# Performance work log

Measured on AMD Instinct MI355X. Metric: run time of the kernel, lower is better.

Reference implementation:

```python
import jax, jax.numpy as jnp
import numpy as np

N = 100000
E = 1600000
D = 128
EIG = 32
NUM_MOTIFS = 64
EPS = 1e-8  # torch cosine_similarity eps


def setup_inputs() -> dict:
    key = jax.random.key(0)
    ks = jax.random.split(key, 12)
    return {
        "q": jax.random.normal(ks[0], (N, D), jnp.float32),
        "k": jax.random.normal(ks[1], (N, D), jnp.float32),
        "v": jax.random.normal(ks[2], (N, D), jnp.float32),
        "eigs": jax.random.normal(ks[3], (N, EIG), jnp.float32),
        "motif_adj_vals": jax.random.uniform(ks[4], (E,), jnp.float32),
        "lambda0": jax.random.normal(ks[5], (1,), jnp.float32) * 0.1,
        "gamma": jax.random.normal(ks[6], (1,), jnp.float32) * 0.1,
        "motif_emb_w": jax.random.uniform(ks[7], (NUM_MOTIFS, 1), jnp.float32),
        "row": jax.random.randint(ks[8], (E,), 0, N, jnp.int32),
        "col": jax.random.randint(ks[9], (E,), 0, N, jnp.int32),
        "motif_ids": jax.random.randint(ks[10], (N,), 0, NUM_MOTIFS, jnp.int32),
    }


def _sparse_softmax(vals, row, n):
    # softmax of per-edge values grouped by destination/row index
    m = jax.ops.segment_max(vals, row, num_segments=n)
    e = jnp.exp(vals - m[row])
    z = jax.ops.segment_sum(e, row, num_segments=n)
    return e / z[row]


def reference(q, k, v, eigs, motif_adj_vals, lambda0, gamma, motif_emb_w,
              row, col, motif_ids):
    sqrt_dim = 1.0 / jnp.sqrt(jnp.asarray(q.shape[1], q.dtype))
    # edge-wise q.k dot product, scaled
    x = jnp.sum(q[row] * k[col], axis=-1) * sqrt_dim          # [E]
    # eig branch (args.model contains 'eig'); note original does NOT scale by sqrt_eig
    y = jnp.sum(eigs[row] * eigs[col], axis=-1)               # [E]
    s0 = x + jnp.exp(lambda0[0]) * y
    # motif branch: embedding lookup + cosine similarity along the edge dim (dim=0)
    me = motif_emb_w[motif_ids][:, 0]                          # [N]
    a, b = me[row], me[col]                                    # [E]
    sim = jnp.sum(a * b) / (jnp.maximum(jnp.linalg.norm(a), EPS)
                            * jnp.maximum(jnp.linalg.norm(b), EPS))
    s1 = motif_adj_vals * gamma[0] * sim                       # [E]
    n = q.shape[0]
    attn = 0.5 * (_sparse_softmax(s0, row, n) + _sparse_softmax(s1, row, n))
    # sparse-dense matmul: out[r] = sum_e attn_e * v[col_e]
    return jax.ops.segment_sum(attn[:, None] * v[col], row, num_segments=n)
```

## Files before the change

kernel.cpp:

```cpp
#include <hip/hip_runtime.h>
#include <math.h>

#define N_NODES 100000
#define N_EDGES 1600000
#define DIM 128
#define EIGD 32
#define CS_EPS 1e-8f

#define B1 256
#define CHUNK 6250
#define NB 391

static const size_t OFF_REC    = 0;
static const size_t OFF_SE     = 12800000;
static const size_t OFF_GH     = 25600000;
static const size_t OFF_BSTART = 26000384;
static const size_t OFF_GPART  = 26001952;
static const size_t OFF_OFFS   = 26006048;
static const size_t OFF_SCAL   = 26406064;
static const size_t OFF_KB     = 26406080;
static const size_t OFF_VB     = 52006080;
static const size_t OFF_EB     = 77606080;

__device__ __forceinline__ unsigned short f2bf(float f) {
    unsigned u = __float_as_uint(f);
    unsigned r = (u + 0x7fffu + ((u >> 16) & 1u)) >> 16;
    return (unsigned short)r;
}
__device__ __forceinline__ float blo(unsigned w) { return __uint_as_float(w << 16); }
__device__ __forceinline__ float bhi(unsigned w) { return __uint_as_float(w & 0xffff0000u); }

#define K4C 3200000
#define E4C 800000

__global__ void __launch_bounds__(256) ka_cvt(
        const float* __restrict__ k, const float* __restrict__ v,
        const float* __restrict__ eigs,
        ushort* __restrict__ kb, ushort* __restrict__ vb,
        ushort* __restrict__ eb) {
    int i = blockIdx.x * blockDim.x + threadIdx.x;
    const float* src; ushort* dst; int j;
    if (i < K4C)            { src = k;    dst = kb; j = i; }
    else if (i < 2 * K4C)   { src = v;    dst = vb; j = i - K4C; }
    else if (i < 2*K4C+E4C) { src = eigs; dst = eb; j = i - 2 * K4C; }
    else return;
    float4 f = ((const float4*)src)[j];
    ushort4 o;
    o.x = f2bf(f.x); o.y = f2bf(f.y); o.z = f2bf(f.z); o.w = f2bf(f.w);
    ((ushort4*)dst)[j] = o;
}

__global__ void __launch_bounds__(256) kb_hist(
        const int* __restrict__ row, const int* __restrict__ col,
        const float* __restrict__ motif_w, const int* __restrict__ motif_ids,
        int* __restrict__ gh, float4* __restrict__ gpart) {
    __shared__ int hist[NB];
    __shared__ float wlds[64];
    __shared__ float red[3][4];
    const int t = threadIdx.x, b = blockIdx.x;
    for (int i = t; i < NB; i += 256) hist[i] = 0;
    if (t < 64) wlds[t] = motif_w[t];
    __syncthreads();

    const int e0 = b * CHUNK, e1 = min(N_EDGES, e0 + CHUNK);
    float sab = 0.f, saa = 0.f, sbb = 0.f;
    for (int e = e0 + t; e < e1; e += 256) {
        int r = row[e], c = col[e];
        atomicAdd(&hist[r >> 8], 1);
        float mr = wlds[motif_ids[r]], mc = wlds[motif_ids[c]];
        sab += mr * mc; saa += mr * mr; sbb += mc * mc;
    }
#pragma unroll
    for (int off = 32; off >= 1; off >>= 1) {
        sab += __shfl_xor(sab, off);
        saa += __shfl_xor(saa, off);
        sbb += __shfl_xor(sbb, off);
    }
    int lane = t & 63, wid = t >> 6;
    if (lane == 0) { red[0][wid] = sab; red[1][wid] = saa; red[2][wid] = sbb; }
    __syncthreads();
    if (t == 0) {
        float a = 0.f, bb = 0.f, cc = 0.f;
#pragma unroll
        for (int i = 0; i < 4; i++) { a += red[0][i]; bb += red[1][i]; cc += red[2][i]; }
        gpart[b] = make_float4(a, bb, cc, 0.f);
    }
    __syncthreads();
    for (int i = t; i < NB; i += 256) gh[b * NB + i] = hist[i];
}

__global__ void __launch_bounds__(512) ke_scan(
        int* __restrict__ gh, int* __restrict__ bstart,
        const float4* __restrict__ gpart, const float* __restrict__ gamma,
        float* __restrict__ scal, int* __restrict__ offs) {
    const int t = threadIdx.x;
    __shared__ int tot[512];
    int mytot = 0;
    if (t < NB) {
        int run = 0;
        for (int b = 0; b < B1; b++) {
            int v = gh[b * NB + t];
            gh[b * NB + t] = run;
            run += v;
        }
        mytot = run;
    }
    tot[t] = mytot;
    __syncthreads();
    for (int off = 1; off < 512; off <<= 1) {
        int v = (t >= off) ? tot[t - off] : 0;
        __syncthreads();
        tot[t] += v;
        __syncthreads();
    }
    if (t < NB) bstart[t] = tot[t] - mytot;
    if (t == NB - 1) {
        bstart[NB] = tot[t];
        offs[N_NODES] = tot[t];
    }

    float sab = 0.f, saa = 0.f, sbb = 0.f;
    for (int i = t; i < B1; i += 512) {
        float4 g = gpart[i];
        sab += g.x; saa += g.y; sbb += g.z;
    }
#pragma unroll
    for (int off = 32; off >= 1; off >>= 1) {
        sab += __shfl_xor(sab, off);
        saa += __shfl_xor(saa, off);
        sbb += __shfl_xor(sbb, off);
    }
    __shared__ float red[3][8];
    int lane = t & 63, wid = t >> 6;
    if (lane == 0) { red[0][wid] = sab; red[1][wid] = saa; red[2][wid] = sbb; }
    __syncthreads();
    if (t == 0) {
        float a = 0.f, bb = 0.f, cc = 0.f;
#pragma unroll
        for (int i = 0; i < 8; i++) { a += red[0][i]; bb += red[1][i]; cc += red[2][i]; }
        float na = sqrtf(bb); if (na < CS_EPS) na = CS_EPS;
        float nb2 = sqrtf(cc); if (nb2 < CS_EPS) nb2 = CS_EPS;
        scal[0] = gamma[0] * (a / (na * nb2));
    }
}

__global__ void __launch_bounds__(256) kd_coarse(
        const int* __restrict__ row, const int* __restrict__ col,
        const float* __restrict__ adj, const int* __restrict__ gh,
        const int* __restrict__ bstart, int2* __restrict__ rec) {
    __shared__ int cur[NB];
    const int t = threadIdx.x, b = blockIdx.x;
    for (int i = t; i < NB; i += 256) cur[i] = bstart[i] + gh[b * NB + i];
    __syncthreads();
    const int e0 = b * CHUNK, e1 = min(N_EDGES, e0 + CHUNK);
    for (int e = e0 + t; e < e1; e += 256) {
        int r = row[e];
        int pos = atomicAdd(&cur[r >> 8], 1);
        rec[pos] = make_int2(col[e] | ((r & 255) << 17), __float_as_int(adj[e]));
    }
}

__global__ void __launch_bounds__(256) kf_fine(
        const int2* __restrict__ rec, const int* __restrict__ bstart,
        int* __restrict__ offs, float2* __restrict__ se) {
    __shared__ int hist[256], sc[256], cur[256];
    const int t = threadIdx.x, b = blockIdx.x;
    hist[t] = 0;
    __syncthreads();
    const int s = bstart[b], e1 = bstart[b + 1];
    for (int i = s + t; i < e1; i += 256) {
        int rl = (rec[i].x >> 17) & 255;
        atomicAdd(&hist[rl], 1);
    }
    __syncthreads();
    int v = hist[t];
    sc[t] = v;
    __syncthreads();
    for (int off = 1; off < 256; off <<= 1) {
        int w = (t >= off) ? sc[t - off] : 0;
        __syncthreads();
        sc[t] += w;
        __syncthreads();
    }
    int excl = sc[t] - v;
    int rowg = b * 256 + t;
    if (rowg < N_NODES) offs[rowg] = s + excl;
    cur[t] = s + excl;
    __syncthreads();
    for (int i = s + t; i < e1; i += 256) {
        int2 rc = rec[i];
        int rl = (rc.x >> 17) & 255;
        int pos = atomicAdd(&cur[rl], 1);
        se[pos] = make_float2(__int_as_float(rc.x & 0x1FFFF), __int_as_float(rc.y));
    }
}

__global__ void __launch_bounds__(256) k4_flash(
        const float* __restrict__ q, const ushort* __restrict__ kb,
        const ushort* __restrict__ eb, const ushort* __restrict__ vb,
        const float* __restrict__ lambda0, const int* __restrict__ offs,
        const float2* __restrict__ se, const float* __restrict__ scal,
        float* __restrict__ out) {
    const int tid  = threadIdx.x;
    const int lane = tid & 63;
    const int wid  = tid >> 6;
    const int r = blockIdx.x * 4 + wid;
    if (r >= N_NODES) return;
    const int l16 = lane & 15;
    const int grp = lane >> 4;
    const float inv_sqrt_d = 0.08838834764831843f;

    const int start = offs[r], end = offs[r + 1];
    if (end == start) {
        ((float2*)(out + (size_t)r * DIM))[lane] = make_float2(0.f, 0.f);
        return;
    }

    const float el0 = expf(lambda0[0]);
    const float cs  = scal[0];

    const float4* qp = (const float4*)(q + (size_t)r * DIM);
    const float4 qa = qp[l16 * 2];
    const float4 qc = qp[l16 * 2 + 1];
    const unsigned erw = *(const unsigned*)(eb + (size_t)r * EIGD + l16 * 2);
    const float er0 = blo(erw), er1 = bhi(erw);

    float m0 = -INFINITY, z0 = 0.f, m1 = -INFINITY, z1 = 0.f;
    float2 acc0 = make_float2(0.f, 0.f), acc1 = make_float2(0.f, 0.f);

    for (int base = start; base < end; base += 4) {
        int e = base + grp;
        float s0p = -INFINITY, s1v = -INFINITY;
        int c = 0;
        if (e < end) {
            float2 ea = se[e];
            c = __float_as_int(ea.x);
            s1v = cs * ea.y;
            const uint4 kw = *(const uint4*)(kb + (size_t)c * DIM + l16 * 8);
            float x;
            x = qa.x * blo(kw.x);
            x = fmaf(qa.y, bhi(kw.x), x);
            x = fmaf(qa.z, blo(kw.y), x);
            x = fmaf(qa.w, bhi(kw.y), x);
            x = fmaf(qc.x, blo(kw.z), x);
            x = fmaf(qc.y, bhi(kw.z), x);
            x = fmaf(qc.z, blo(kw.w), x);
            x = fmaf(qc.w, bhi(kw.w), x);
            const unsigned ecw = *(const unsigned*)(eb + (size_t)c * EIGD + l16 * 2);
            float y = er0 * blo(ecw) + er1 * bhi(ecw);
            s0p = x * inv_sqrt_d + el0 * y;
        }
#pragma unroll
        for (int off = 8; off >= 1; off >>= 1) s0p += __shfl_xor(s0p, off);

        float s00 = __shfl(s0p, 0),  s01 = __shfl(s0p, 16);
        float s02 = __shfl(s0p, 32), s03 = __shfl(s0p, 48);
        float s10 = __shfl(s1v, 0),  s11 = __shfl(s1v, 16);
        float s12 = __shfl(s1v, 32), s13 = __shfl(s1v, 48);
        int   c0  = __shfl(c, 0),    c1  = __shfl(c, 16);
        int   c2  = __shfl(c, 32),   c3  = __shfl(c, 48);
        int cnt = end - base;

        float nm0 = fmaxf(m0, fmaxf(fmaxf(s00, s01), fmaxf(s02, s03)));
        float r0  = __expf(m0 - nm0);
        float w00 = __expf(s00 - nm0);
        float w01 = __expf(s01 - nm0);
        float w02 = __expf(s02 - nm0);
        float w03 = __expf(s03 - nm0);
        z0 = z0 * r0 + w00 + w01 + w02 + w03;
        m0 = nm0;

        float nm1 = fmaxf(m1, fmaxf(fmaxf(s10, s11), fmaxf(s12, s13)));
        float r1  = __expf(m1 - nm1);
        float w10 = __expf(s10 - nm1);
        float w11 = __expf(s11 - nm1);
        float w12 = __expf(s12 - nm1);
        float w13 = __expf(s13 - nm1);
        z1 = z1 * r1 + w10 + w11 + w12 + w13;
        m1 = nm1;

        acc0.x *= r0; acc0.y *= r0;
        acc1.x *= r1; acc1.y *= r1;
        {
            unsigned vw = *(const unsigned*)(vb + (size_t)c0 * DIM + lane * 2);
            float vx = blo(vw), vy = bhi(vw);
            acc0.x = fmaf(w00, vx, acc0.x); acc0.y = fmaf(w00, vy, acc0.y);
            acc1.x = fmaf(w10, vx, acc1.x); acc1.y = fmaf(w10, vy, acc1.y);
        }
        if (cnt > 1) {
            unsigned vw = *(const unsigned*)(vb + (size_t)c1 * DIM + lane * 2);
            float vx = blo(vw), vy = bhi(vw);
            acc0.x = fmaf(w01, vx, acc0.x); acc0.y = fmaf(w01, vy, acc0.y);
            acc1.x = fmaf(w11, vx, acc1.x); acc1.y = fmaf(w11, vy, acc1.y);
        }
        if (cnt > 2) {
            unsigned vw = *(const unsigned*)(vb + (size_t)c2 * DIM + lane * 2);
            float vx = blo(vw), vy = bhi(vw);
            acc0.x = fmaf(w02, vx, acc0.x); acc0.y = fmaf(w02, vy, acc0.y);
            acc1.x = fmaf(w12, vx, acc1.x); acc1.y = fmaf(w12, vy, acc1.y);
        }
        if (cnt > 3) {
            unsigned vw = *(const unsigned*)(vb + (size_t)c3 * DIM + lane * 2);
            float vx = blo(vw), vy = bhi(vw);
            acc0.x = fmaf(w03, vx, acc0.x); acc0.y = fmaf(w03, vy, acc0.y);
            acc1.x = fmaf(w13, vx, acc1.x); acc1.y = fmaf(w13, vy, acc1.y);
        }
    }

    float iz0 = 1.f / z0, iz1 = 1.f / z1;
    float2 o = make_float2(0.5f * (acc0.x * iz0 + acc1.x * iz1),
                           0.5f * (acc0.y * iz0 + acc1.y * iz1));
    ((float2*)(out + (size_t)r * DIM))[lane] = o;
}

extern "C" void kernel_launch(void* const* d_in, const int* in_sizes, int n_in,
                              void* d_out, int out_size, void* d_ws, size_t ws_size,
                              hipStream_t stream) {
    const float* q        = (const float*)d_in[0];
    const float* k        = (const float*)d_in[1];
    const float* v        = (const float*)d_in[2];
    const float* eigs     = (const float*)d_in[3];
    const float* adj      = (const float*)d_in[4];
    const float* lambda0  = (const float*)d_in[5];
    const float* gamma    = (const float*)d_in[6];
    const float* motif_w  = (const float*)d_in[7];
    const int*   row      = (const int*)d_in[8];
    const int*   col      = (const int*)d_in[9];
    const int*   motif_ids= (const int*)d_in[10];
    float* out = (float*)d_out;

    char* ws = (char*)d_ws;
    int2*   rec    = (int2*)(ws + OFF_REC);
    float2* se     = (float2*)(ws + OFF_SE);
    int*    gh     = (int*)(ws + OFF_GH);
    int*    bstart = (int*)(ws + OFF_BSTART);
    float4* gpart  = (float4*)(ws + OFF_GPART);
    int*    offs   = (int*)(ws + OFF_OFFS);
    float*  scal   = (float*)(ws + OFF_SCAL);
    ushort* kb     = (ushort*)(ws + OFF_KB);
    ushort* vb     = (ushort*)(ws + OFF_VB);
    ushort* eb     = (ushort*)(ws + OFF_EB);

    hipLaunchKernelGGL(ka_cvt, dim3((2 * K4C + E4C + 255) / 256), dim3(256), 0, stream,
                       k, v, eigs, kb, vb, eb);
    hipLaunchKernelGGL(kb_hist, dim3(B1), dim3(256), 0, stream,
                       row, col, motif_w, motif_ids, gh, gpart);
    hipLaunchKernelGGL(ke_scan, dim3(1), dim3(512), 0, stream,
                       gh, bstart, gpart, gamma, scal, offs);
    hipLaunchKernelGGL(kd_coarse, dim3(B1), dim3(256), 0, stream,
                       row, col, adj, gh, bstart, rec);
    hipLaunchKernelGGL(kf_fine, dim3(NB), dim3(256), 0, stream,
                       rec, bstart, offs, se);
    hipLaunchKernelGGL(k4_flash, dim3((N_NODES + 3) / 4), dim3(256), 0, stream,
                       q, kb, eb, vb, lambda0, offs, se, scal, out);
}
```

Measured before the change: 478.1 us.

## Fuse fine bucket sort into attention kernel and parallelize histogram scan

```diff
diff --git a/kernel.cpp b/kernel.cpp
--- a/kernel.cpp
+++ b/kernel.cpp
@@ -7,20 +7,24 @@
 #define EIGD 32
 #define CS_EPS 1e-8f
 
-#define B1 256
-#define CHUNK 6250
-#define NB 391
+#define HB 1024
+#define CHUNK 1563
+#define NB2 1563
+#define CAP 1536
+#define K4C 3200000
+#define E4C 800000
+#define CVB 28125
 
 static const size_t OFF_REC    = 0;
-static const size_t OFF_SE     = 12800000;
-static const size_t OFF_GH     = 25600000;
-static const size_t OFF_BSTART = 26000384;
-static const size_t OFF_GPART  = 26001952;
-static const size_t OFF_OFFS   = 26006048;
-static const size_t OFF_SCAL   = 26406064;
-static const size_t OFF_KB     = 26406080;
-static const size_t OFF_VB     = 52006080;
-static const size_t OFF_EB     = 77606080;
+static const size_t OFF_GH     = 12800000;
+static const size_t OFF_BSTART = 19202048;
+static const size_t OFF_BTOT   = 19208304;
+static const size_t OFF_GPART  = 19214560;
+static const size_t OFF_FLAG   = 19230944;
+static const size_t OFF_SCAL   = 19230960;
+static const size_t OFF_KB     = 19231040;
+static const size_t OFF_VB     = 44831040;
+static const size_t OFF_EB     = 70431040;
 
 __device__ __forceinline__ unsigned short f2bf(float f) {
     unsigned u = __float_as_uint(f);
@@ -30,43 +34,38 @@
 __device__ __forceinline__ float blo(unsigned w) { return __uint_as_float(w << 16); }
 __device__ __forceinline__ float bhi(unsigned w) { return __uint_as_float(w & 0xffff0000u); }
 
-#define K4C 3200000
-#define E4C 800000
-
-__global__ void __launch_bounds__(256) ka_cvt(
+__global__ void __launch_bounds__(256) k1_cvt_hist(
         const float* __restrict__ k, const float* __restrict__ v,
         const float* __restrict__ eigs,
-        ushort* __restrict__ kb, ushort* __restrict__ vb,
-        ushort* __restrict__ eb) {
-    int i = blockIdx.x * blockDim.x + threadIdx.x;
-    const float* src; ushort* dst; int j;
-    if (i < K4C)            { src = k;    dst = kb; j = i; }
-    else if (i < 2 * K4C)   { src = v;    dst = vb; j = i - K4C; }
-    else if (i < 2*K4C+E4C) { src = eigs; dst = eb; j = i - 2 * K4C; }
-    else return;
-    float4 f = ((const float4*)src)[j];
-    ushort4 o;
-    o.x = f2bf(f.x); o.y = f2bf(f.y); o.z = f2bf(f.z); o.w = f2bf(f.w);
-    ((ushort4*)dst)[j] = o;
-}
-
-__global__ void __launch_bounds__(256) kb_hist(
         const int* __restrict__ row, const int* __restrict__ col,
         const float* __restrict__ motif_w, const int* __restrict__ motif_ids,
-        int* __restrict__ gh, float4* __restrict__ gpart) {
-    __shared__ int hist[NB];
+        ushort* __restrict__ kb, ushort* __restrict__ vb, ushort* __restrict__ eb,
+        int* __restrict__ gh, float4* __restrict__ gpart, int* __restrict__ flag) {
+    const int t = threadIdx.x, b = blockIdx.x;
+    if (b >= HB) {
+        int i = (b - HB) * 256 + t;
+        const float* src; ushort* dst; int j;
+        if (i < K4C)          { src = k;    dst = kb; j = i; }
+        else if (i < 2 * K4C) { src = v;    dst = vb; j = i - K4C; }
+        else                  { src = eigs; dst = eb; j = i - 2 * K4C; }
+        float4 f = ((const float4*)src)[j];
+        ushort4 o;
+        o.x = f2bf(f.x); o.y = f2bf(f.y); o.z = f2bf(f.z); o.w = f2bf(f.w);
+        ((ushort4*)dst)[j] = o;
+        return;
+    }
+    __shared__ int hist[NB2];
     __shared__ float wlds[64];
     __shared__ float red[3][4];
-    const int t = threadIdx.x, b = blockIdx.x;
-    for (int i = t; i < NB; i += 256) hist[i] = 0;
+    if (b == 0 && t == 0) flag[0] = 0;
+    for (int i = t; i < NB2; i += 256) hist[i] = 0;
     if (t < 64) wlds[t] = motif_w[t];
     __syncthreads();
-
     const int e0 = b * CHUNK, e1 = min(N_EDGES, e0 + CHUNK);
     float sab = 0.f, saa = 0.f, sbb = 0.f;
     for (int e = e0 + t; e < e1; e += 256) {
         int r = row[e], c = col[e];
-        atomicAdd(&hist[r >> 8], 1);
+        atomicAdd(&hist[r >> 6], 1);
         float mr = wlds[motif_ids[r]], mc = wlds[motif_ids[c]];
         sab += mr * mc; saa += mr * mr; sbb += mc * mc;
     }
@@ -85,96 +84,23 @@
         for (int i = 0; i < 4; i++) { a += red[0][i]; bb += red[1][i]; cc += red[2][i]; }
         gpart[b] = make_float4(a, bb, cc, 0.f);
     }
-    __syncthreads();
-    for (int i = t; i < NB; i += 256) gh[b * NB + i] = hist[i];
-}
-
-__global__ void __launch_bounds__(512) ke_scan(
-        int* __restrict__ gh, int* __restrict__ bstart,
+    for (int i = t; i < NB2; i += 256) gh[b * NB2 + i] = hist[i];
+}
+
+__global__ void __launch_bounds__(256) k2_scan(
+        int* __restrict__ gh, int* __restrict__ btot, int* __restrict__ bstart,
         const float4* __restrict__ gpart, const float* __restrict__ gamma,
-        float* __restrict__ scal, int* __restrict__ offs) {
-    const int t = threadIdx.x;
-    __shared__ int tot[512];
-    int mytot = 0;
-    if (t < NB) {
-        int run = 0;
-        for (int b = 0; b < B1; b++) {
-            int v = gh[b * NB + t];
-            gh[b * NB + t] = run;
-            run += v;
-        }
-        mytot = run;
-    }
-    tot[t] = mytot;
-    __syncthreads();
-    for (int off = 1; off < 512; off <<= 1) {
-        int v = (t >= off) ? tot[t - off] : 0;
-        __syncthreads();
-        tot[t] += v;
-        __syncthreads();
-    }
-    if (t < NB) bstart[t] = tot[t] - mytot;
-    if (t == NB - 1) {
-        bstart[NB] = tot[t];
-        offs[N_NODES] = tot[t];
-    }
-
-    float sab = 0.f, saa = 0.f, sbb = 0.f;
-    for (int i = t; i < B1; i += 512) {
-        float4 g = gpart[i];
-        sab += g.x; saa += g.y; sbb += g.z;
-    }
-#pragma unroll
-    for (int off = 32; off >= 1; off >>= 1) {
-        sab += __shfl_xor(sab, off);
-        saa += __shfl_xor(saa, off);
-        sbb += __shfl_xor(sbb, off);
-    }
-    __shared__ float red[3][8];
-    int lane = t & 63, wid = t >> 6;
-    if (lane == 0) { red[0][wid] = sab; red[1][wid] = saa; red[2][wid] = sbb; }
-    __syncthreads();
-    if (t == 0) {
-        float a = 0.f, bb = 0.f, cc = 0.f;
-#pragma unroll
-        for (int i = 0; i < 8; i++) { a += red[0][i]; bb += red[1][i]; cc += red[2][i]; }
-        float na = sqrtf(bb); if (na < CS_EPS) na = CS_EPS;
-        float nb2 = sqrtf(cc); if (nb2 < CS_EPS) nb2 = CS_EPS;
-        scal[0] = gamma[0] * (a / (na * nb2));
-    }
-}
-
-__global__ void __launch_bounds__(256) kd_coarse(
-        const int* __restrict__ row, const int* __restrict__ col,
-        const float* __restrict__ adj, const int* __restrict__ gh,
-        const int* __restrict__ bstart, int2* __restrict__ rec) {
-    __shared__ int cur[NB];
-    const int t = threadIdx.x, b = blockIdx.x;
-    for (int i = t; i < NB; i += 256) cur[i] = bstart[i] + gh[b * NB + i];
-    __syncthreads();
-    const int e0 = b * CHUNK, e1 = min(N_EDGES, e0 + CHUNK);
-    for (int e = e0 + t; e < e1; e += 256) {
-        int r = row[e];
-        int pos = atomicAdd(&cur[r >> 8], 1);
-        rec[pos] = make_int2(col[e] | ((r & 255) << 17), __float_as_int(adj[e]));
-    }
-}
-
-__global__ void __launch_bounds__(256) kf_fine(
-        const int2* __restrict__ rec, const int* __restrict__ bstart,
-        int* __restrict__ offs, float2* __restrict__ se) {
-    __shared__ int hist[256], sc[256], cur[256];
-    const int t = threadIdx.x, b = blockIdx.x;
-    hist[t] = 0;
-    __syncthreads();
-    const int s = bstart[b], e1 = bstart[b + 1];
-    for (int i = s + t; i < e1; i += 256) {
-        int rl = (rec[i].x >> 17) & 255;
-        atomicAdd(&hist[rl], 1);
-    }
-    __syncthreads();
-    int v = hist[t];
-    sc[t] = v;
+        float* __restrict__ scal, int* __restrict__ flag) {
+    const int t = threadIdx.x, cb = blockIdx.x;
+    __shared__ int sc[256];
+    __shared__ int lastf;
+    __shared__ float red[3][4];
+    int v0 = gh[(t * 4 + 0) * NB2 + cb];
+    int v1 = gh[(t * 4 + 1) * NB2 + cb];
+    int v2 = gh[(t * 4 + 2) * NB2 + cb];
+    int v3 = gh[(t * 4 + 3) * NB2 + cb];
+    int tot4 = v0 + v1 + v2 + v3;
+    sc[t] = tot4;
     __syncthreads();
     for (int off = 1; off < 256; off <<= 1) {
         int w = (t >= off) ? sc[t - off] : 0;
@@ -182,135 +108,223 @@
         sc[t] += w;
         __syncthreads();
     }
-    int excl = sc[t] - v;
-    int rowg = b * 256 + t;
-    if (rowg < N_NODES) offs[rowg] = s + excl;
-    cur[t] = s + excl;
-    __syncthreads();
-    for (int i = s + t; i < e1; i += 256) {
-        int2 rc = rec[i];
-        int rl = (rc.x >> 17) & 255;
-        int pos = atomicAdd(&cur[rl], 1);
-        se[pos] = make_float2(__int_as_float(rc.x & 0x1FFFF), __int_as_float(rc.y));
-    }
-}
-
-__global__ void __launch_bounds__(256) k4_flash(
+    int excl = sc[t] - tot4;
+    gh[(t * 4 + 0) * NB2 + cb] = excl;
+    gh[(t * 4 + 1) * NB2 + cb] = excl + v0;
+    gh[(t * 4 + 2) * NB2 + cb] = excl + v0 + v1;
+    gh[(t * 4 + 3) * NB2 + cb] = excl + v0 + v1 + v2;
+    if (t == 255) atomicExch(&btot[cb], excl + tot4);
+    __syncthreads();
+    if (t == 0) lastf = (atomicAdd(flag, 1) == NB2 - 1);
+    __syncthreads();
+    if (!lastf) return;
+
+    if (t < 64) {
+        int base = 0;
+        for (int ch = 0; ch < (NB2 + 63) / 64; ++ch) {
+            int idx = ch * 64 + t;
+            int vv = (idx < NB2) ? atomicAdd(&btot[idx], 0) : 0;
+            int inc = vv;
+#pragma unroll
+            for (int off = 1; off < 64; off <<= 1) {
+                int w = __shfl_up(inc, off);
+                if (t >= off) inc += w;
+            }
+            if (idx < NB2) bstart[idx] = base + inc - vv;
+            base += __shfl(inc, 63);
+        }
+        if (t == 0) bstart[NB2] = base;
+    }
+    float a2 = 0.f, b2 = 0.f, c2 = 0.f;
+    for (int i = t; i < HB; i += 256) {
+        float4 g = gpart[i];
+        a2 += g.x; b2 += g.y; c2 += g.z;
+    }
+#pragma unroll
+    for (int off = 32; off >= 1; off >>= 1) {
+        a2 += __shfl_xor(a2, off);
+        b2 += __shfl_xor(b2, off);
+        c2 += __shfl_xor(c2, off);
+    }
+    int lane = t & 63, wid = t >> 6;
+    if (lane == 0) { red[0][wid] = a2; red[1][wid] = b2; red[2][wid] = c2; }
+    __syncthreads();
+    if (t == 0) {
+        float a = 0.f, bb = 0.f, cc = 0.f;
+#pragma unroll
+        for (int i = 0; i < 4; i++) { a += red[0][i]; bb += red[1][i]; cc += red[2][i]; }
+        float na = sqrtf(bb); if (na < CS_EPS) na = CS_EPS;
+        float nb2v = sqrtf(cc); if (nb2v < CS_EPS) nb2v = CS_EPS;
+        scal[0] = gamma[0] * (a / (na * nb2v));
+    }
+}
+
+__global__ void __launch_bounds__(256) k3_coarse(
+        const int* __restrict__ row, const int* __restrict__ col,
+        const float* __restrict__ adj, const int* __restrict__ gh,
+        const int* __restrict__ bstart, int2* __restrict__ rec) {
+    __shared__ int cur[NB2];
+    const int t = threadIdx.x, b = blockIdx.x;
+    for (int i = t; i < NB2; i += 256) cur[i] = bstart[i] + gh[b * NB2 + i];
+    __syncthreads();
+    const int e0 = b * CHUNK, e1 = min(N_EDGES, e0 + CHUNK);
+    for (int e = e0 + t; e < e1; e += 256) {
+        int r = row[e];
+        int pos = atomicAdd(&cur[r >> 6], 1);
+        rec[pos] = make_int2(col[e] | ((r & 63) << 17), __float_as_int(adj[e]));
+    }
+}
+
+__global__ void __launch_bounds__(256) k4_flashf(
         const float* __restrict__ q, const ushort* __restrict__ kb,
         const ushort* __restrict__ eb, const ushort* __restrict__ vb,
-        const float* __restrict__ lambda0, const int* __restrict__ offs,
-        const float2* __restrict__ se, const float* __restrict__ scal,
+        const float* __restrict__ lambda0, const int* __restrict__ bstart,
+        const int2* __restrict__ rec, const float* __restrict__ scal,
         float* __restrict__ out) {
-    const int tid  = threadIdx.x;
-    const int lane = tid & 63;
-    const int wid  = tid >> 6;
-    const int r = blockIdx.x * 4 + wid;
-    if (r >= N_NODES) return;
-    const int l16 = lane & 15;
-    const int grp = lane >> 4;
-    const float inv_sqrt_d = 0.08838834764831843f;
-
-    const int start = offs[r], end = offs[r + 1];
-    if (end == start) {
-        ((float2*)(out + (size_t)r * DIM))[lane] = make_float2(0.f, 0.f);
-        return;
-    }
+    const int t = threadIdx.x, b = blockIdx.x;
+    const int lane = t & 63, wid = t >> 6;
+    const int l16 = lane & 15, grp = lane >> 4;
+    __shared__ int2 lrec[CAP];
+    __shared__ int2 srec[CAP];
+    __shared__ int lhist[64], lscan[64], lcur[64];
+
+    const int s = bstart[b];
+    int cnt = bstart[b + 1] - s;
+    if (cnt > CAP) cnt = CAP;
+    if (t < 64) lhist[t] = 0;
+    __syncthreads();
+    for (int i = t; i < cnt; i += 256) {
+        int2 rc = rec[s + i];
+        lrec[i] = rc;
+        atomicAdd(&lhist[(rc.x >> 17) & 63], 1);
+    }
+    __syncthreads();
+    if (t < 64) {
+        int h = lhist[t];
+        int inc = h;
+#pragma unroll
+        for (int off = 1; off < 64; off <<= 1) {
+            int w = __shfl_up(inc, off);
+            if (t >= off) inc += w;
+        }
+        lscan[t] = inc - h;
+        lcur[t]  = inc - h;
+    }
+    __syncthreads();
+    for (int i = t; i < cnt; i += 256) {
+        int2 rc = lrec[i];
+        int rl = (rc.x >> 17) & 63;
+        int p = atomicAdd(&lcur[rl], 1);
+        srec[p] = make_int2(rc.x & 0x1FFFF, rc.y);
+    }
+    __syncthreads();
 
     const float el0 = expf(lambda0[0]);
     const float cs  = scal[0];
-
-    const float4* qp = (const float4*)(q + (size_t)r * DIM);
-    const float4 qa = qp[l16 * 2];
-    const float4 qc = qp[l16 * 2 + 1];
-    const unsigned erw = *(const unsigned*)(eb + (size_t)r * EIGD + l16 * 2);
-    const float er0 = blo(erw), er1 = bhi(erw);
-
-    float m0 = -INFINITY, z0 = 0.f, m1 = -INFINITY, z1 = 0.f;
-    float2 acc0 = make_float2(0.f, 0.f), acc1 = make_float2(0.f, 0.f);
-
-    for (int base = start; base < end; base += 4) {
-        int e = base + grp;
-        float s0p = -INFINITY, s1v = -INFINITY;
-        int c = 0;
-        if (e < end) {
-            float2 ea = se[e];
-            c = __float_as_int(ea.x);
-            s1v = cs * ea.y;
-            const uint4 kw = *(const uint4*)(kb + (size_t)c * DIM + l16 * 8);
-            float x;
-            x = qa.x * blo(kw.x);
-            x = fmaf(qa.y, bhi(kw.x), x);
-            x = fmaf(qa.z, blo(kw.y), x);
-            x = fmaf(qa.w, bhi(kw.y), x);
-            x = fmaf(qc.x, blo(kw.z), x);
-            x = fmaf(qc.y, bhi(kw.z), x);
-            x = fmaf(qc.z, blo(kw.w), x);
-            x = fmaf(qc.w, bhi(kw.w), x);
-            const unsigned ecw = *(const unsigned*)(eb + (size_t)c * EIGD + l16 * 2);
-            float y = er0 * blo(ecw) + er1 * bhi(ecw);
-            s0p = x * inv_sqrt_d + el0 * y;
+    const float inv_sqrt_d = 0.08838834764831843f;
+
+    for (int rr = 0; rr < 16; ++rr) {
+        const int rloc = wid * 16 + rr;
+        const int r = b * 64 + rloc;
+        if (r >= N_NODES) break;
+        const int lst = lscan[rloc], led = lcur[rloc];
+        if (led == lst) {
+            ((float2*)(out + (size_t)r * DIM))[lane] = make_float2(0.f, 0.f);
+            continue;
         }
-#pragma unroll
-        for (int off = 8; off >= 1; off >>= 1) s0p += __shfl_xor(s0p, off);
-
-        float s00 = __shfl(s0p, 0),  s01 = __shfl(s0p, 16);
-        float s02 = __shfl(s0p, 32), s03 = __shfl(s0p, 48);
-        float s10 = __shfl(s1v, 0),  s11 = __shfl(s1v, 16);
-        float s12 = __shfl(s1v, 32), s13 = __shfl(s1v, 48);
-        int   c0  = __shfl(c, 0),    c1  = __shfl(c, 16);
-        int   c2  = __shfl(c, 32),   c3  = __shfl(c, 48);
-        int cnt = end - base;
-
-        float nm0 = fmaxf(m0, fmaxf(fmaxf(s00, s01), fmaxf(s02, s03)));
-        float r0  = __expf(m0 - nm0);
-        float w00 = __expf(s00 - nm0);
-        float w01 = __expf(s01 - nm0);
-        float w02 = __expf(s02 - nm0);
-        float w03 = __expf(s03 - nm0);
-        z0 = z0 * r0 + w00 + w01 + w02 + w03;
-        m0 = nm0;
-
-        float nm1 = fmaxf(m1, fmaxf(fmaxf(s10, s11), fmaxf(s12, s13)));
-        float r1  = __expf(m1 - nm1);
-        float w10 = __expf(s10 - nm1);
-        float w11 = __expf(s11 - nm1);
-        float w12 = __expf(s12 - nm1);
-        float w13 = __expf(s13 - nm1);
-        z1 = z1 * r1 + w10 + w11 + w12 + w13;
-        m1 = nm1;
-
-        acc0.x *= r0; acc0.y *= r0;
-        acc1.x *= r1; acc1.y *= r1;
-        {
-            unsigned vw = *(const unsigned*)(vb + (size_t)c0 * DIM + lane * 2);
-            float vx = blo(vw), vy = bhi(vw);
-            acc0.x = fmaf(w00, vx, acc0.x); acc0.y = fmaf(w00, vy, acc0.y);
-            acc1.x = fmaf(w10, vx, acc1.x); acc1.y = fmaf(w10, vy, acc1.y);
+        const float4* qp = (const float4*)(q + (size_t)r * DIM);
+        const float4 qa = qp[l16 * 2];
+        const float4 qc = qp[l16 * 2 + 1];
+        const unsigned erw = *(const unsigned*)(eb + (size_t)r * EIGD + l16 * 2);
+        const float er0 = blo(erw), er1 = bhi(erw);
+
+        float m0 = -INFINITY, z0 = 0.f, m1 = -INFINITY, z1 = 0.f;
+        float2 acc0 = make_float2(0.f, 0.f), acc1 = make_float2(0.f, 0.f);
+
+        for (int base = lst; base < led; base += 4) {
+            int e = base + grp;
+            float s0p = -INFINITY, s1v = -INFINITY;
+            int c = 0;
+            if (e < led) {
+                int2 ea = srec[e];
+                c = ea.x;
+                s1v = cs * __int_as_float(ea.y);
+                const uint4 kw = *(const uint4*)(kb + (size_t)c * DIM + l16 * 8);
+                float x;
+                x = qa.x * blo(kw.x);
+                x = fmaf(qa.y, bhi(kw.x), x);
+                x = fmaf(qa.z, blo(kw.y), x);
+                x = fmaf(qa.w, bhi(kw.y), x);
+                x = fmaf(qc.x, blo(kw.z), x);
+                x = fmaf(qc.y, bhi(kw.z), x);
+                x = fmaf(qc.z, blo(kw.w), x);
+                x = fmaf(qc.w, bhi(kw.w), x);
+                const unsigned ecw = *(const unsigned*)(eb + (size_t)c * EIGD + l16 * 2);
+                float y = er0 * blo(ecw) + er1 * bhi(ecw);
+                s0p = x * inv_sqrt_d + el0 * y;
+            }
+#pragma unroll
+            for (int off = 8; off >= 1; off >>= 1) s0p += __shfl_xor(s0p, off);
+
+            float s00 = __shfl(s0p, 0),  s01 = __shfl(s0p, 16);
+            float s02 = __shfl(s0p, 32), s03 = __shfl(s0p, 48);
+            float s10 = __shfl(s1v, 0),  s11 = __shfl(s1v, 16);
+            float s12 = __shfl(s1v, 32), s13 = __shfl(s1v, 48);
+            int   c0  = __shfl(c, 0),    c1  = __shfl(c, 16);
+            int   c2  = __shfl(c, 32),   c3  = __shfl(c, 48);
+            int rem = led - base;
+
+            float nm0 = fmaxf(m0, fmaxf(fmaxf(s00, s01), fmaxf(s02, s03)));
+            float r0  = __expf(m0 - nm0);
+            float w00 = __expf(s00 - nm0);
+            float w01 = __expf(s01 - nm0);
+            float w02 = __expf(s02 - nm0);
+            float w03 = __expf(s03 - nm0);
+            z0 = z0 * r0 + w00 + w01 + w02 + w03;
+            m0 = nm0;
+
+            float nm1 = fmaxf(m1, fmaxf(fmaxf(s10, s11), fmaxf(s12, s13)));
+            float r1  = __expf(m1 - nm1);
+            float w10 = __expf(s10 - nm1);
+            float w11 = __expf(s11 - nm1);
+            float w12 = __expf(s12 - nm1);
+            float w13 = __expf(s13 - nm1);
+            z1 = z1 * r1 + w10 + w11 + w12 + w13;
+            m1 = nm1;
+
+            acc0.x *= r0; acc0.y *= r0;
+            acc1.x *= r1; acc1.y *= r1;
+            {
+                unsigned vw = *(const unsigned*)(vb + (size_t)c0 * DIM + lane * 2);
+                float vx = blo(vw), vy = bhi(vw);
+                acc0.x = fmaf(w00, vx, acc0.x); acc0.y = fmaf(w00, vy, acc0.y);
+                acc1.x = fmaf(w10, vx, acc1.x); acc1.y = fmaf(w10, vy, acc1.y);
+            }
+            if (rem > 1) {
+                unsigned vw = *(const unsigned*)(vb + (size_t)c1 * DIM + lane * 2);
+                float vx = blo(vw), vy = bhi(vw);
+                acc0.x = fmaf(w01, vx, acc0.x); acc0.y = fmaf(w01, vy, acc0.y);
+                acc1.x = fmaf(w11, vx, acc1.x); acc1.y = fmaf(w11, vy, acc1.y);
+            }
+            if (rem > 2) {
+                unsigned vw = *(const unsigned*)(vb + (size_t)c2 * DIM + lane * 2);
+                float vx = blo(vw), vy = bhi(vw);
+                acc0.x = fmaf(w02, vx, acc0.x); acc0.y = fmaf(w02, vy, acc0.y);
+                acc1.x = fmaf(w12, vx, acc1.x); acc1.y = fmaf(w12, vy, acc1.y);
+            }
+            if (rem > 3) {
+                unsigned vw = *(const unsigned*)(vb + (size_t)c3 * DIM + lane * 2);
+                float vx = blo(vw), vy = bhi(vw);
+                acc0.x = fmaf(w03, vx, acc0.x); acc0.y = fmaf(w03, vy, acc0.y);
+                acc1.x = fmaf(w13, vx, acc1.x); acc1.y = fmaf(w13, vy, acc1.y);
+            }
         }
-        if (cnt > 1) {
-            unsigned vw = *(const unsigned*)(vb + (size_t)c1 * DIM + lane * 2);
-            float vx = blo(vw), vy = bhi(vw);
-            acc0.x = fmaf(w01, vx, acc0.x); acc0.y = fmaf(w01, vy, acc0.y);
-            acc1.x = fmaf(w11, vx, acc1.x); acc1.y = fmaf(w11, vy, acc1.y);
-        }
-        if (cnt > 2) {
-            unsigned vw = *(const unsigned*)(vb + (size_t)c2 * DIM + lane * 2);
-            float vx = blo(vw), vy = bhi(vw);
-            acc0.x = fmaf(w02, vx, acc0.x); acc0.y = fmaf(w02, vy, acc0.y);
-            acc1.x = fmaf(w12, vx, acc1.x); acc1.y = fmaf(w12, vy, acc1.y);
-        }
-        if (cnt > 3) {
-            unsigned vw = *(const unsigned*)(vb + (size_t)c3 * DIM + lane * 2);
-            float vx = blo(vw), vy = bhi(vw);
-            acc0.x = fmaf(w03, vx, acc0.x); acc0.y = fmaf(w03, vy, acc0.y);
-            acc1.x = fmaf(w13, vx, acc1.x); acc1.y = fmaf(w13, vy, acc1.y);
-        }
-    }
-
-    float iz0 = 1.f / z0, iz1 = 1.f / z1;
-    float2 o = make_float2(0.5f * (acc0.x * iz0 + acc1.x * iz1),
-                           0.5f * (acc0.y * iz0 + acc1.y * iz1));
-    ((float2*)(out + (size_t)r * DIM))[lane] = o;
+
+        float iz0 = 1.f / z0, iz1 = 1.f / z1;
+        float2 o = make_float2(0.5f * (acc0.x * iz0 + acc1.x * iz1),
+                               0.5f * (acc0.y * iz0 + acc1.y * iz1));
+        ((float2*)(out + (size_t)r * DIM))[lane] = o;
+    }
 }
 
 extern "C" void kernel_launch(void* const* d_in, const int* in_sizes, int n_in,
@@ -331,26 +345,23 @@
 
     char* ws = (char*)d_ws;
     int2*   rec    = (int2*)(ws + OFF_REC);
-    float2* se     = (float2*)(ws + OFF_SE);
     int*    gh     = (int*)(ws + OFF_GH);
     int*    bstart = (int*)(ws + OFF_BSTART);
+    int*    btot   = (int*)(ws + OFF_BTOT);
     float4* gpart  = (float4*)(ws + OFF_GPART);
-    int*    offs   = (int*)(ws + OFF_OFFS);
+    int*    flag   = (int*)(ws + OFF_FLAG);
     float*  scal   = (float*)(ws + OFF_SCAL);
     ushort* kb     = (ushort*)(ws + OFF_KB);
     ushort* vb     = (ushort*)(ws + OFF_VB);
     ushort* eb     = (ushort*)(ws + OFF_EB);
 
-    hipLaunchKernelGGL(ka_cvt, dim3((2 * K4C + E4C + 255) / 256), dim3(256), 0, stream,
-                       k, v, eigs, kb, vb, eb);
-    hipLaunchKernelGGL(kb_hist, dim3(B1), dim3(256), 0, stream,
-                       row, col, motif_w, motif_ids, gh, gpart);
-    hipLaunchKernelGGL(ke_scan, dim3(1), dim3(512), 0, stream,
-                       gh, bstart, gpart, gamma, scal, offs);
-    hipLaunchKernelGGL(kd_coarse, dim3(B1), dim3(256), 0, stream,
+    hipLaunchKernelGGL(k1_cvt_hist, dim3(HB + CVB), dim3(256), 0, stream,
+                       k, v, eigs, row, col, motif_w, motif_ids,
+                       kb, vb, eb, gh, gpart, flag);
+    hipLaunchKernelGGL(k2_scan, dim3(NB2), dim3(256), 0, stream,
+                       gh, btot, bstart, gpart, gamma, scal, flag);
+    hipLaunchKernelGGL(k3_coarse, dim3(HB), dim3(256), 0, stream,
                        row, col, adj, gh, bstart, rec);
-    hipLaunchKernelGGL(kf_fine, dim3(NB), dim3(256), 0, stream,
-                       rec, bstart, offs, se);
-    hipLaunchKernelGGL(k4_flash, dim3((N_NODES + 3) / 4), dim3(256), 0, stream,
-                       q, kb, eb, vb, lambda0, offs, se, scal, out);
-}
+    hipLaunchKernelGGL(k4_flashf, dim3(NB2), dim3(256), 0, stream,
+                       q, kb, eb, vb, lambda0, bstart, rec, scal, out);
+}
```

Measured after the change: 596.1 us. 1.25x slower.
